# Kernel tuning notes

Measured on AMD Instinct MI355X. Metric: run time of the kernel, lower is better.

The kernel has to match this reference:

```python
import jax, jax.numpy as jnp
import numpy as np

NEG = -10000.0


def _build_label_vocab():
    vocab = {'O': 0}
    i = 1
    for t in ['PER', 'ORG', 'LOC', 'MISC']:
        for p in ['B', 'I', 'E', 'S']:
            vocab[f'{p}-{t}'] = i
            i += 1
    return vocab


def _init_transition(key):
    """Random transition with BIOES constraints, matching CRF.initialize()."""
    vocab = _build_label_vocab()
    L = len(vocab) + 2          # 19 (17 labels + start + end)
    start, end = L - 2, L - 1
    T = np.array(jax.random.normal(key, (L, L)), dtype=np.float32)
    T[:, end] = NEG
    T[start, :] = NEG
    for lf, i_f in vocab.items():
        pf, tf = ('O', 'O') if lf == 'O' else lf.split('-')
        for lt, i_t in vocab.items():
            pt, tt = ('O', 'O') if lt == 'O' else lt.split('-')
            allowed = (pf in ('O', 'E', 'S') and pt in ('O', 'B', 'S')) or \
                      (pf in ('B', 'I') and pt in ('I', 'E') and tf == tt)
            if not allowed:
                T[i_t, i_f] = NEG
    return jnp.asarray(T)


def setup_inputs() -> dict:
    key = jax.random.key(0)
    k1, k2, k3, k4 = jax.random.split(key, 4)
    B, S, NL = 4096, 256, 17
    logits = jax.random.normal(k1, (B, S, NL), dtype=jnp.float32)
    labels = jax.random.randint(k2, (B, S), 0, NL)
    lens = jax.random.randint(k3, (B,), 1, S + 1)   # lengths in [1, S]
    transition = _init_transition(k4)                # [19, 19]
    return {"logits": logits, "labels": labels, "lens": lens,
            "transition": transition}


def reference(logits, labels, lens, transition):
    """CRF log-likelihood: gold_score(pad_logits(logits)) - norm_score."""
    B, S, NL = logits.shape
    L = transition.shape[0]       # label_size = NL + 2
    start, end = L - 2, L - 1

    # pad_logits: append start/end columns with -10000
    pads = jnp.full((B, S, 2), NEG, dtype=logits.dtype)
    logits_p = jnp.concatenate([logits, pads], axis=2)   # [B, S, L]

    tmask = (jnp.arange(S)[None, :] < lens[:, None])     # [B, S] valid tokens

    # ---- gold score ----
    # unary: gather emission score of the gold label at each position
    unary = jnp.take_along_axis(logits_p, labels[:, :, None], axis=2)[:, :, 0]
    unary = (unary * tmask.astype(logits.dtype)).sum(axis=1)

    # binary: transition scores along the gold path (with start/end padding)
    labels_ext = jnp.concatenate(
        [jnp.full((B, 1), start, labels.dtype), labels,
         jnp.full((B, 1), end, labels.dtype)], axis=1)   # [B, S+2]
    emask = jnp.arange(S + 2)[None, :] < (lens + 1)[:, None]
    labels_ext = jnp.where(emask, labels_ext, end)
    trn_scr = transition[labels_ext[:, 1:], labels_ext[:, :-1]]  # [B, S+1]
    bmask = (jnp.arange(S + 1)[None, :] < (lens + 1)[:, None]).astype(logits.dtype)
    binary = (trn_scr * bmask).sum(axis=1)

    gold = unary + binary

    # ---- partition (norm) score: forward algorithm over time ----
    alpha0 = jnp.full((B, L), NEG, dtype=logits.dtype).at[:, start].set(0.0)

    def step(alpha, xs):
        logit, m = xs  # logit: [B, L], m: [B] bool (position < len)
        # alpha_nxt[b,i] = logit[b,i] + LSE_j(alpha[b,j] + T[i,j])
        nxt = logit + jax.nn.logsumexp(alpha[:, None, :] + transition[None], axis=2)
        alpha = jnp.where(m[:, None], nxt, alpha)
        return alpha, None

    alpha, _ = jax.lax.scan(step, alpha0,
                            (jnp.swapaxes(logits_p, 0, 1), tmask.T))
    alpha = alpha + transition[end][None, :]
    norm = jax.nn.logsumexp(alpha, axis=1)

    return gold - norm   # [B] per-sequence log-likelihood
```

## Files before the change

kernel.cpp:

```cpp
#include <hip/hip_runtime.h>

constexpr int S    = 256;
constexpr int NL   = 17;
constexpr int L    = 19;
constexpr int CAPB = 16384;

typedef float v4 __attribute__((ext_vector_type(4), aligned(4)));

__device__ float g_Z[CAPB * 17];
__device__ float g_V[CAPB * 17];
__device__ float g_mf[CAPB];
__device__ float g_mv[CAPB];

__host__ __device__ constexpr bool allowedTo(int i, int j) {
    const int pi = (i == 0) ? 4 : ((i - 1) & 3);
    const int pj = (j == 0) ? 4 : ((j - 1) & 3);
    const int ti = (i == 0) ? -1 : ((i - 1) >> 2);
    const int tj = (j == 0) ? -2 : ((j - 1) >> 2);
    const bool fromOES = (pj == 4) || (pj == 2) || (pj == 3);
    const bool toOBS   = (pi == 4) || (pi == 0) || (pi == 3);
    if (fromOES && toOBS) return true;
    if (((pj == 0) || (pj == 1)) && ((pi == 1) || (pi == 2)) && (ti == tj)) return true;
    return false;
}

#define STEP(T_, CUR, NXT, RN)                                              \
    {                                                                       \
        const int t_ = (T_);                                                \
        {                                                                   \
            const int o_ = tokoff(t_ + 1);                                  \
            const v4   l0 = *(const v4*)(base + o_);                        \
            const v4   l1 = *(const v4*)(base + o_ + 16);                   \
            const v4   l2 = *(const v4*)(base + o_ + 32);                   \
            const v4   l3 = *(const v4*)(base + o_ + 48);                   \
            const float l4 = *(const float*)(base + o_ + 64);               \
            NXT[0] = l0.x;  NXT[1] = l0.y;  NXT[2] = l0.z;  NXT[3] = l0.w;  \
            NXT[4] = l1.x;  NXT[5] = l1.y;  NXT[6] = l1.z;  NXT[7] = l1.w;  \
            NXT[8] = l2.x;  NXT[9] = l2.y;  NXT[10] = l2.z; NXT[11] = l2.w; \
            NXT[12] = l3.x; NXT[13] = l3.y; NXT[14] = l3.z; NXT[15] = l3.w; \
            NXT[16] = l4;                                                   \
        }                                                                   \
        float q[17];                                                        \
        _Pragma("unroll")                                                   \
        for (int j = 0; j < 17; ++j) q[j] = __expf(CUR[j]) * p[j];          \
        _Pragma("unroll")                                                   \
        for (int i = 0; i < 17; ++i) {                                      \
            float acc = 0.0f;                                               \
            bool  fst = true;                                               \
            _Pragma("unroll")                                               \
            for (int j = 0; j < 17; ++j) {                                  \
                const bool al = BWD ? allowedTo(j, i) : allowedTo(i, j);    \
                if (al) {                                                   \
                    acc = fst ? cf[i][j] * q[j]                             \
                              : fmaf(cf[i][j], q[j], acc);                  \
                    fst = false;                                            \
                }                                                           \
            }                                                               \
            p[i] = acc;                                                     \
        }                                                                   \
        if (RN) {                                                           \
            float mx = p[16];                                               \
            _Pragma("unroll")                                               \
            for (int i = 0; i < 16; i += 2)                                 \
                mx = fmaxf(mx, fmaxf(p[i], p[i + 1]));                      \
            const float r_ = __frcp_rn(mx);                                 \
            _Pragma("unroll")                                               \
            for (int i = 0; i < 17; ++i) p[i] *= r_;                        \
            m += __logf(mx);                                                \
        }                                                                   \
        if (t_ == nup - 1) {                                                \
            float* dst = SC + bc * 17;                                      \
            _Pragma("unroll")                                               \
            for (int i = 0; i < 17; ++i) dst[i] = p[i];                     \
            SM[bc] = m;                                                     \
        }                                                                   \
    }

template <bool BWD>
__device__ __forceinline__ void chain(const float* __restrict__ logits,
                                      const int*   __restrict__ lens,
                                      const float* __restrict__ T,
                                      int B, int z)
{
    const int  lane  = threadIdx.x;
    const int  braw  = z * 64 + lane;
    const bool valid = braw < B;
    const int  bc    = valid ? braw : 0;

    const int len = lens[bc];
    const int mid = len >> 1;
    int nup = BWD ? (len - 1 - mid) : mid;
    if (!valid) nup = 0;

    float cf[17][17];
    #pragma unroll
    for (int i = 0; i < 17; ++i)
        #pragma unroll
        for (int j = 0; j < 17; ++j) {
            const bool al = BWD ? allowedTo(j, i) : allowedTo(i, j);
            if (al) cf[i][j] = __expf(BWD ? T[j * L + i] : T[i * L + j]);
        }

    float p[17];
    #pragma unroll
    for (int i = 0; i < 17; ++i)
        p[i] = __expf(BWD ? T[(L - 1) * L + i] : T[i * L + (L - 2)]);

    float m = 0.0f;

    float* SC = BWD ? g_V : g_Z;
    float* SM = BWD ? g_mv : g_mf;

    if (nup == 0 && valid) {
        float* dst = SC + bc * 17;
        #pragma unroll
        for (int i = 0; i < 17; ++i) dst[i] = p[i];
        SM[bc] = 0.0f;
    }

    int nmax = nup;
    #pragma unroll
    for (int o = 32; o >= 1; o >>= 1) nmax = max(nmax, __shfl_xor(nmax, o));

    const char* base = (const char*)logits;
    const int   sb4  = bc * (S * NL * 4);

    auto tokoff = [&](int t) -> int {
        int tok = BWD ? (len - 1 - t) : t;
        if (BWD) tok = tok > 0 ? tok : 0;
        return sb4 + tok * (NL * 4);
    };

    float curv[17], nxtv[17];
    {
        const int o_ = tokoff(0);
        const v4   l0 = *(const v4*)(base + o_);
        const v4   l1 = *(const v4*)(base + o_ + 16);
        const v4   l2 = *(const v4*)(base + o_ + 32);
        const v4   l3 = *(const v4*)(base + o_ + 48);
        const float l4 = *(const float*)(base + o_ + 64);
        curv[0] = l0.x;  curv[1] = l0.y;  curv[2] = l0.z;  curv[3] = l0.w;
        curv[4] = l1.x;  curv[5] = l1.y;  curv[6] = l1.z;  curv[7] = l1.w;
        curv[8] = l2.x;  curv[9] = l2.y;  curv[10] = l2.z; curv[11] = l2.w;
        curv[12] = l3.x; curv[13] = l3.y; curv[14] = l3.z; curv[15] = l3.w;
        curv[16] = l4;
    }

    for (int tb = 0; tb < nmax; tb += 2) {
        STEP(tb,     curv, nxtv, false)
        STEP(tb + 1, nxtv, curv, ((tb & 3) == 2))
    }
}

__global__ __launch_bounds__(64, 1)
void crf_chain(const float* __restrict__ logits, const int* __restrict__ lens,
               const float* __restrict__ T, int B, int nbh)
{
    if ((int)blockIdx.x < nbh) chain<false>(logits, lens, T, B, blockIdx.x);
    else                       chain<true >(logits, lens, T, B, blockIdx.x - nbh);
}

__global__ __launch_bounds__(64)
void crf_combine(const float* __restrict__ logits, const int* __restrict__ labels,
                 const int* __restrict__ lens, const float* __restrict__ T,
                 float* __restrict__ out, int B)
{
    const int b    = blockIdx.x;
    const int wtid = threadIdx.x;
    const int len  = lens[b];
    const int mid  = len >> 1;

    float prod = 0.0f;
    if (wtid < 17) {
        const float z  = g_Z[b * 17 + wtid];
        const float v  = g_V[b * 17 + wtid];
        const float lg = logits[(size_t)b * (S * NL) + mid * NL + wtid];
        prod = z * v * __expf(lg);
    }
    #pragma unroll
    for (int o = 32; o >= 1; o >>= 1) prod += __shfl_xor(prod, o);
    const float norm = g_mf[b] + g_mv[b] + __logf(prod);

    const int* labp = labels + b * S;
    float gsum = 0.0f;
    for (int c = 0; c < len; c += 64) {
        const int tok = c + wtid;
        if (tok < len) {
            const int lab = labp[tok];
            const int prv = (tok == 0) ? (L - 2) : labp[tok - 1];
            gsum += logits[(size_t)b * (S * NL) + tok * NL + lab] + T[lab * L + prv];
        }
    }
    #pragma unroll
    for (int o = 32; o >= 1; o >>= 1) gsum += __shfl_xor(gsum, o);
    const float gold = gsum + T[(L - 1) * L + labp[len - 1]];

    if (wtid == 0) out[b] = gold - norm;
}

extern "C" void kernel_launch(void* const* d_in, const int* in_sizes, int n_in,
                              void* d_out, int out_size, void* d_ws, size_t ws_size,
                              hipStream_t stream)
{
    (void)n_in; (void)out_size; (void)d_ws; (void)ws_size;
    const float* logits     = (const float*)d_in[0];
    const int*   labels     = (const int*)d_in[1];
    const int*   lens       = (const int*)d_in[2];
    const float* transition = (const float*)d_in[3];
    float*       out        = (float*)d_out;
    const int B   = in_sizes[2];
    const int NBH = (B + 63) / 64;

    crf_chain<<<dim3(2 * NBH), dim3(64), 0, stream>>>(logits, lens, transition, B, NBH);
    crf_combine<<<dim3(B), dim3(64), 0, stream>>>(logits, labels, lens, transition, out, B);
}
```

Measured before the change: 166.5 us.

## Deepen logits prefetch to four tokens and hand-expand sparse CRF matvec

The forward and backward chain kernels now keep four token slots of logits in flight, which raises prefetch depth from one token to four so global load latency is hidden behind the serial recurrence. The sparse BIOES matvec is written out explicitly through macros and uses balanced tree additions in place of a serial FMA chain, which shortens each step's dependency chain. Renormalisation now runs once every four steps, and nmax is rounded up to a multiple of four. The cost is much higher register pressure from four slots plus the coefficients, and some extra padded iterations, with backward offsets clamped at the sequence start.

```diff
diff --git a/kernel.cpp b/kernel.cpp
--- a/kernel.cpp
+++ b/kernel.cpp
@@ -12,152 +12,197 @@
 __device__ float g_mf[CAPB];
 __device__ float g_mv[CAPB];
 
-__host__ __device__ constexpr bool allowedTo(int i, int j) {
-    const int pi = (i == 0) ? 4 : ((i - 1) & 3);
-    const int pj = (j == 0) ? 4 : ((j - 1) & 3);
-    const int ti = (i == 0) ? -1 : ((i - 1) >> 2);
-    const int tj = (j == 0) ? -2 : ((j - 1) >> 2);
-    const bool fromOES = (pj == 4) || (pj == 2) || (pj == 3);
-    const bool toOBS   = (pi == 4) || (pi == 0) || (pi == 3);
-    if (fromOES && toOBS) return true;
-    if (((pj == 0) || (pj == 1)) && ((pi == 1) || (pi == 2)) && (ti == tj)) return true;
-    return false;
-}
-
-#define STEP(T_, CUR, NXT, RN)                                              \
-    {                                                                       \
-        const int t_ = (T_);                                                \
-        {                                                                   \
-            const int o_ = tokoff(t_ + 1);                                  \
-            const v4   l0 = *(const v4*)(base + o_);                        \
-            const v4   l1 = *(const v4*)(base + o_ + 16);                   \
-            const v4   l2 = *(const v4*)(base + o_ + 32);                   \
-            const v4   l3 = *(const v4*)(base + o_ + 48);                   \
-            const float l4 = *(const float*)(base + o_ + 64);               \
-            NXT[0] = l0.x;  NXT[1] = l0.y;  NXT[2] = l0.z;  NXT[3] = l0.w;  \
-            NXT[4] = l1.x;  NXT[5] = l1.y;  NXT[6] = l1.z;  NXT[7] = l1.w;  \
-            NXT[8] = l2.x;  NXT[9] = l2.y;  NXT[10] = l2.z; NXT[11] = l2.w; \
-            NXT[12] = l3.x; NXT[13] = l3.y; NXT[14] = l3.z; NXT[15] = l3.w; \
-            NXT[16] = l4;                                                   \
-        }                                                                   \
-        float q[17];                                                        \
-        _Pragma("unroll")                                                   \
-        for (int j = 0; j < 17; ++j) q[j] = __expf(CUR[j]) * p[j];          \
-        _Pragma("unroll")                                                   \
-        for (int i = 0; i < 17; ++i) {                                      \
-            float acc = 0.0f;                                               \
-            bool  fst = true;                                               \
-            _Pragma("unroll")                                               \
-            for (int j = 0; j < 17; ++j) {                                  \
-                const bool al = BWD ? allowedTo(j, i) : allowedTo(i, j);    \
-                if (al) {                                                   \
-                    acc = fst ? cf[i][j] * q[j]                             \
-                              : fmaf(cf[i][j], q[j], acc);                  \
-                    fst = false;                                            \
-                }                                                           \
-            }                                                               \
-            p[i] = acc;                                                     \
-        }                                                                   \
-        if (RN) {                                                           \
-            float mx = p[16];                                               \
-            _Pragma("unroll")                                               \
-            for (int i = 0; i < 16; i += 2)                                 \
-                mx = fmaxf(mx, fmaxf(p[i], p[i + 1]));                      \
-            const float r_ = __frcp_rn(mx);                                 \
-            _Pragma("unroll")                                               \
-            for (int i = 0; i < 17; ++i) p[i] *= r_;                        \
-            m += __logf(mx);                                                \
-        }                                                                   \
-        if (t_ == nup - 1) {                                                \
-            float* dst = SC + bc * 17;                                      \
-            _Pragma("unroll")                                               \
-            for (int i = 0; i < 17; ++i) dst[i] = p[i];                     \
-            SM[bc] = m;                                                     \
-        }                                                                   \
-    }
-
-template <bool BWD>
-__device__ __forceinline__ void chain(const float* __restrict__ logits,
-                                      const int*   __restrict__ lens,
-                                      const float* __restrict__ T,
-                                      int B, int z)
+#define ROWF(X,i) X(i,0) X(i,3) X(i,4) X(i,7) X(i,8) X(i,11) X(i,12) X(i,15) X(i,16)
+#define FWD_ALL(X) \
+  ROWF(X,0) ROWF(X,1) ROWF(X,4) ROWF(X,5) ROWF(X,8) ROWF(X,9) ROWF(X,12) ROWF(X,13) ROWF(X,16) \
+  X(2,1) X(2,2) X(3,1) X(3,2) X(6,5) X(6,6) X(7,5) X(7,6) \
+  X(10,9) X(10,10) X(11,9) X(11,10) X(14,13) X(14,14) X(15,13) X(15,14)
+
+#define ROWB(X,i) X(i,0) X(i,1) X(i,4) X(i,5) X(i,8) X(i,9) X(i,12) X(i,13) X(i,16)
+#define BWD_ALL(X) \
+  ROWB(X,0) ROWB(X,3) ROWB(X,4) ROWB(X,7) ROWB(X,8) ROWB(X,11) ROWB(X,12) ROWB(X,15) ROWB(X,16) \
+  X(1,2) X(1,3) X(2,2) X(2,3) X(5,6) X(5,7) X(6,6) X(6,7) \
+  X(9,10) X(9,11) X(10,10) X(10,11) X(13,14) X(13,15) X(14,14) X(14,15)
+
+#define APPLY17(X) X(0) X(1) X(2) X(3) X(4) X(5) X(6) X(7) X(8) X(9) X(10) X(11) X(12) X(13) X(14) X(15) X(16)
+
+#define DCF_F(i,j) const float cf_##i##_##j = __expf(Tg[(i)*19+(j)]);
+#define DCF_B(i,j) const float cf_##i##_##j = __expf(Tg[(j)*19+(i)]);
+
+#define DPF(i) float p##i = __expf(Tg[(i)*19+17]);
+#define DPB(i) float p##i = __expf(Tg[18*19+(i)]);
+
+#define DECLSLOT(T) float T##0,T##1,T##2,T##3,T##4,T##5,T##6,T##7,T##8,T##9, \
+                          T##10,T##11,T##12,T##13,T##14,T##15,T##16;
+
+#define LOADTOK(T, OFF) { \
+    const char* a_ = base + (OFF); \
+    const v4 x0_ = *(const v4*)(a_); \
+    const v4 x1_ = *(const v4*)(a_ + 16); \
+    const v4 x2_ = *(const v4*)(a_ + 32); \
+    const v4 x3_ = *(const v4*)(a_ + 48); \
+    const float x4_ = *(const float*)(a_ + 64); \
+    T##0=x0_.x; T##1=x0_.y; T##2=x0_.z; T##3=x0_.w; \
+    T##4=x1_.x; T##5=x1_.y; T##6=x1_.z; T##7=x1_.w; \
+    T##8=x2_.x; T##9=x2_.y; T##10=x2_.z; T##11=x2_.w; \
+    T##12=x3_.x; T##13=x3_.y; T##14=x3_.z; T##15=x3_.w; T##16=x4_; }
+
+#define MKQALL(T) \
+    const float q0 = __expf(T##0) * p0;   const float q1 = __expf(T##1) * p1; \
+    const float q2 = __expf(T##2) * p2;   const float q3 = __expf(T##3) * p3; \
+    const float q4 = __expf(T##4) * p4;   const float q5 = __expf(T##5) * p5; \
+    const float q6 = __expf(T##6) * p6;   const float q7 = __expf(T##7) * p7; \
+    const float q8 = __expf(T##8) * p8;   const float q9 = __expf(T##9) * p9; \
+    const float q10 = __expf(T##10) * p10; const float q11 = __expf(T##11) * p11; \
+    const float q12 = __expf(T##12) * p12; const float q13 = __expf(T##13) * p13; \
+    const float q14 = __expf(T##14) * p14; const float q15 = __expf(T##15) * p15; \
+    const float q16 = __expf(T##16) * p16;
+
+#define FMQ(i,j) cf_##i##_##j * q##j
+#define ROW9N(i,a,b,c,d,e,f,g,h,k) \
+    const float n##i = (((FMQ(i,a)+FMQ(i,b)) + (FMQ(i,c)+FMQ(i,d))) + \
+                        ((FMQ(i,e)+FMQ(i,f)) + (FMQ(i,g)+FMQ(i,h)))) + FMQ(i,k);
+#define ROW2N(i,a,b) const float n##i = FMQ(i,a) + FMQ(i,b);
+
+#define MATVEC_F \
+    ROW9N(0,0,3,4,7,8,11,12,15,16)  ROW9N(1,0,3,4,7,8,11,12,15,16) \
+    ROW9N(4,0,3,4,7,8,11,12,15,16)  ROW9N(5,0,3,4,7,8,11,12,15,16) \
+    ROW9N(8,0,3,4,7,8,11,12,15,16)  ROW9N(9,0,3,4,7,8,11,12,15,16) \
+    ROW9N(12,0,3,4,7,8,11,12,15,16) ROW9N(13,0,3,4,7,8,11,12,15,16) \
+    ROW9N(16,0,3,4,7,8,11,12,15,16) \
+    ROW2N(2,1,2)   ROW2N(3,1,2)   ROW2N(6,5,6)   ROW2N(7,5,6) \
+    ROW2N(10,9,10) ROW2N(11,9,10) ROW2N(14,13,14) ROW2N(15,13,14)
+
+#define MATVEC_B \
+    ROW9N(0,0,1,4,5,8,9,12,13,16)  ROW9N(3,0,1,4,5,8,9,12,13,16) \
+    ROW9N(4,0,1,4,5,8,9,12,13,16)  ROW9N(7,0,1,4,5,8,9,12,13,16) \
+    ROW9N(8,0,1,4,5,8,9,12,13,16)  ROW9N(11,0,1,4,5,8,9,12,13,16) \
+    ROW9N(12,0,1,4,5,8,9,12,13,16) ROW9N(15,0,1,4,5,8,9,12,13,16) \
+    ROW9N(16,0,1,4,5,8,9,12,13,16) \
+    ROW2N(1,2,3)   ROW2N(2,2,3)   ROW2N(5,6,7)   ROW2N(6,6,7) \
+    ROW2N(9,10,11) ROW2N(10,10,11) ROW2N(13,14,15) ROW2N(14,14,15)
+
+#define ASG(i)  p##i = n##i;
+#define ASGR(i) p##i = n##i * r_;
+
+#define STORE_P { \
+    float* d_ = SC + bc * 17; \
+    d_[0]=p0; d_[1]=p1; d_[2]=p2; d_[3]=p3; d_[4]=p4; d_[5]=p5; d_[6]=p6; d_[7]=p7; \
+    d_[8]=p8; d_[9]=p9; d_[10]=p10; d_[11]=p11; d_[12]=p12; d_[13]=p13; d_[14]=p14; \
+    d_[15]=p15; d_[16]=p16; \
+    SM[bc] = m; }
+
+#define CHAINSTEP(T, T_, OFFV, RN, MV, DOCLAMP, SSTR) { \
+    MKQALL(T) \
+    OFFV += (SSTR); \
+    if (DOCLAMP) { if (OFFV < capLo) OFFV = capLo; } \
+    LOADTOK(T, OFFV) \
+    MV \
+    if (RN) { \
+        float mxA = fmaxf(fmaxf(n0,n1),  fmaxf(n2,n3)); \
+        float mxB = fmaxf(fmaxf(n4,n5),  fmaxf(n6,n7)); \
+        float mxC = fmaxf(fmaxf(n8,n9),  fmaxf(n10,n11)); \
+        float mxD = fmaxf(fmaxf(n12,n13),fmaxf(n14,n15)); \
+        float mx  = fmaxf(fmaxf(fmaxf(mxA,mxB), fmaxf(mxC,mxD)), n16); \
+        const float r_ = __frcp_rn(mx); \
+        m += __logf(mx); \
+        APPLY17(ASGR) \
+    } else { \
+        APPLY17(ASG) \
+    } \
+    if ((T_) == nup - 1) STORE_P \
+}
+
+__device__ __forceinline__ void chainF(const float* __restrict__ logits,
+                                       const int* __restrict__ lens,
+                                       const float* __restrict__ Tg, int B, int z)
 {
     const int  lane  = threadIdx.x;
     const int  braw  = z * 64 + lane;
     const bool valid = braw < B;
     const int  bc    = valid ? braw : 0;
-
-    const int len = lens[bc];
-    const int mid = len >> 1;
-    int nup = BWD ? (len - 1 - mid) : mid;
-    if (!valid) nup = 0;
-
-    float cf[17][17];
-    #pragma unroll
-    for (int i = 0; i < 17; ++i)
-        #pragma unroll
-        for (int j = 0; j < 17; ++j) {
-            const bool al = BWD ? allowedTo(j, i) : allowedTo(i, j);
-            if (al) cf[i][j] = __expf(BWD ? T[j * L + i] : T[i * L + j]);
-        }
-
-    float p[17];
-    #pragma unroll
-    for (int i = 0; i < 17; ++i)
-        p[i] = __expf(BWD ? T[(L - 1) * L + i] : T[i * L + (L - 2)]);
-
-    float m = 0.0f;
-
-    float* SC = BWD ? g_V : g_Z;
-    float* SM = BWD ? g_mv : g_mf;
-
-    if (nup == 0 && valid) {
-        float* dst = SC + bc * 17;
-        #pragma unroll
-        for (int i = 0; i < 17; ++i) dst[i] = p[i];
-        SM[bc] = 0.0f;
-    }
+    const int  len   = lens[bc];
+    const int  mid   = len >> 1;
+    const int  nup   = valid ? mid : 0;
+
+    FWD_ALL(DCF_F)
+    APPLY17(DPF)
+    float  m  = 0.0f;
+    float* SC = g_Z;
+    float* SM = g_mf;
+    if (nup == 0 && valid) STORE_P
 
     int nmax = nup;
     #pragma unroll
     for (int o = 32; o >= 1; o >>= 1) nmax = max(nmax, __shfl_xor(nmax, o));
-
-    const char* base = (const char*)logits;
-    const int   sb4  = bc * (S * NL * 4);
-
-    auto tokoff = [&](int t) -> int {
-        int tok = BWD ? (len - 1 - t) : t;
-        if (BWD) tok = tok > 0 ? tok : 0;
-        return sb4 + tok * (NL * 4);
-    };
-
-    float curv[17], nxtv[17];
-    {
-        const int o_ = tokoff(0);
-        const v4   l0 = *(const v4*)(base + o_);
-        const v4   l1 = *(const v4*)(base + o_ + 16);
-        const v4   l2 = *(const v4*)(base + o_ + 32);
-        const v4   l3 = *(const v4*)(base + o_ + 48);
-        const float l4 = *(const float*)(base + o_ + 64);
-        curv[0] = l0.x;  curv[1] = l0.y;  curv[2] = l0.z;  curv[3] = l0.w;
-        curv[4] = l1.x;  curv[5] = l1.y;  curv[6] = l1.z;  curv[7] = l1.w;
-        curv[8] = l2.x;  curv[9] = l2.y;  curv[10] = l2.z; curv[11] = l2.w;
-        curv[12] = l3.x; curv[13] = l3.y; curv[14] = l3.z; curv[15] = l3.w;
-        curv[16] = l4;
-    }
-
-    for (int tb = 0; tb < nmax; tb += 2) {
-        STEP(tb,     curv, nxtv, false)
-        STEP(tb + 1, nxtv, curv, ((tb & 3) == 2))
+    nmax = (nmax + 3) & ~3;
+
+    const char* base  = (const char*)logits;
+    const int   sb4   = bc * (S * NL * 4);
+    const int   capLo = sb4;
+    int off0 = sb4, off1 = sb4 + 68, off2 = sb4 + 136, off3 = sb4 + 204;
+
+    DECLSLOT(sA) DECLSLOT(sB) DECLSLOT(sC) DECLSLOT(sD)
+    LOADTOK(sA, off0) LOADTOK(sB, off1) LOADTOK(sC, off2) LOADTOK(sD, off3)
+
+    for (int tb = 0; tb < nmax; tb += 4) {
+        CHAINSTEP(sA, tb,     off0, 0, MATVEC_F, 0, 272)
+        CHAINSTEP(sB, tb + 1, off1, 0, MATVEC_F, 0, 272)
+        CHAINSTEP(sC, tb + 2, off2, 0, MATVEC_F, 0, 272)
+        CHAINSTEP(sD, tb + 3, off3, 1, MATVEC_F, 0, 272)
+    }
+}
+
+__device__ __forceinline__ void chainB(const float* __restrict__ logits,
+                                       const int* __restrict__ lens,
+                                       const float* __restrict__ Tg, int B, int z)
+{
+    const int  lane  = threadIdx.x;
+    const int  braw  = z * 64 + lane;
+    const bool valid = braw < B;
+    const int  bc    = valid ? braw : 0;
+    const int  len   = lens[bc];
+    const int  mid   = len >> 1;
+    const int  nup   = valid ? (len - 1 - mid) : 0;
+
+    BWD_ALL(DCF_B)
+    APPLY17(DPB)
+    float  m  = 0.0f;
+    float* SC = g_V;
+    float* SM = g_mv;
+    if (nup == 0 && valid) STORE_P
+
+    int nmax = nup;
+    #pragma unroll
+    for (int o = 32; o >= 1; o >>= 1) nmax = max(nmax, __shfl_xor(nmax, o));
+    nmax = (nmax + 3) & ~3;
+
+    const char* base  = (const char*)logits;
+    const int   sb4   = bc * (S * NL * 4);
+    const int   capLo = sb4;
+    const int   t0    = len - 1;
+    int off0 = sb4 + max(t0,     0) * 68;
+    int off1 = sb4 + max(t0 - 1, 0) * 68;
+    int off2 = sb4 + max(t0 - 2, 0) * 68;
+    int off3 = sb4 + max(t0 - 3, 0) * 68;
+
+    DECLSLOT(sA) DECLSLOT(sB) DECLSLOT(sC) DECLSLOT(sD)
+    LOADTOK(sA, off0) LOADTOK(sB, off1) LOADTOK(sC, off2) LOADTOK(sD, off3)
+
+    for (int tb = 0; tb < nmax; tb += 4) {
+        CHAINSTEP(sA, tb,     off0, 0, MATVEC_B, 1, -272)
+        CHAINSTEP(sB, tb + 1, off1, 0, MATVEC_B, 1, -272)
+        CHAINSTEP(sC, tb + 2, off2, 0, MATVEC_B, 1, -272)
+        CHAINSTEP(sD, tb + 3, off3, 1, MATVEC_B, 1, -272)
     }
 }
 
 __global__ __launch_bounds__(64, 1)
 void crf_chain(const float* __restrict__ logits, const int* __restrict__ lens,
-               const float* __restrict__ T, int B, int nbh)
-{
-    if ((int)blockIdx.x < nbh) chain<false>(logits, lens, T, B, blockIdx.x);
-    else                       chain<true >(logits, lens, T, B, blockIdx.x - nbh);
+               const float* __restrict__ Tg, int B, int nbh)
+{
+    if ((int)blockIdx.x < nbh) chainF(logits, lens, Tg, B, blockIdx.x);
+    else                       chainB(logits, lens, Tg, B, blockIdx.x - nbh);
 }
 
 __global__ __launch_bounds__(64)
```

Measured after the change: 168.0 us. About the same (+0.9%).

## Split each CRF chain across two lanes with shuffle-exchanged partial states

Applied to the files above, without the earlier changes.

Each sequence's forward and backward recurrence is now handled by a pair of lanes, each holding 9 of the 17 states. The states are grouped so that only 5 boundary values per lane are exchanged with __shfl_xor each step, and the sparse BIOES transition structure is exploited with small dense A/B blocks and 2-term updates. Loads go through a four-deep rotating slot buffer of per-token logits, and renormalisation happens every four steps. This doubles the number of waves and halves the per-lane serial work and register pressure, at the cost of extra cross-lane shuffles on the critical path.

```diff
diff --git a/kernel.cpp b/kernel.cpp
--- a/kernel.cpp
+++ b/kernel.cpp
@@ -12,152 +12,156 @@
 __device__ float g_mf[CAPB];
 __device__ float g_mv[CAPB];
 
-__host__ __device__ constexpr bool allowedTo(int i, int j) {
-    const int pi = (i == 0) ? 4 : ((i - 1) & 3);
-    const int pj = (j == 0) ? 4 : ((j - 1) & 3);
-    const int ti = (i == 0) ? -1 : ((i - 1) >> 2);
-    const int tj = (j == 0) ? -2 : ((j - 1) >> 2);
-    const bool fromOES = (pj == 4) || (pj == 2) || (pj == 3);
-    const bool toOBS   = (pi == 4) || (pi == 0) || (pi == 3);
-    if (fromOES && toOBS) return true;
-    if (((pj == 0) || (pj == 1)) && ((pi == 1) || (pi == 2)) && (ti == tj)) return true;
-    return false;
-}
-
-#define STEP(T_, CUR, NXT, RN)                                              \
-    {                                                                       \
-        const int t_ = (T_);                                                \
-        {                                                                   \
-            const int o_ = tokoff(t_ + 1);                                  \
-            const v4   l0 = *(const v4*)(base + o_);                        \
-            const v4   l1 = *(const v4*)(base + o_ + 16);                   \
-            const v4   l2 = *(const v4*)(base + o_ + 32);                   \
-            const v4   l3 = *(const v4*)(base + o_ + 48);                   \
-            const float l4 = *(const float*)(base + o_ + 64);               \
-            NXT[0] = l0.x;  NXT[1] = l0.y;  NXT[2] = l0.z;  NXT[3] = l0.w;  \
-            NXT[4] = l1.x;  NXT[5] = l1.y;  NXT[6] = l1.z;  NXT[7] = l1.w;  \
-            NXT[8] = l2.x;  NXT[9] = l2.y;  NXT[10] = l2.z; NXT[11] = l2.w; \
-            NXT[12] = l3.x; NXT[13] = l3.y; NXT[14] = l3.z; NXT[15] = l3.w; \
-            NXT[16] = l4;                                                   \
-        }                                                                   \
-        float q[17];                                                        \
-        _Pragma("unroll")                                                   \
-        for (int j = 0; j < 17; ++j) q[j] = __expf(CUR[j]) * p[j];          \
-        _Pragma("unroll")                                                   \
-        for (int i = 0; i < 17; ++i) {                                      \
-            float acc = 0.0f;                                               \
-            bool  fst = true;                                               \
-            _Pragma("unroll")                                               \
-            for (int j = 0; j < 17; ++j) {                                  \
-                const bool al = BWD ? allowedTo(j, i) : allowedTo(i, j);    \
-                if (al) {                                                   \
-                    acc = fst ? cf[i][j] * q[j]                             \
-                              : fmaf(cf[i][j], q[j], acc);                  \
-                    fst = false;                                            \
-                }                                                           \
-            }                                                               \
-            p[i] = acc;                                                     \
-        }                                                                   \
-        if (RN) {                                                           \
-            float mx = p[16];                                               \
-            _Pragma("unroll")                                               \
-            for (int i = 0; i < 16; i += 2)                                 \
-                mx = fmaxf(mx, fmaxf(p[i], p[i + 1]));                      \
-            const float r_ = __frcp_rn(mx);                                 \
-            _Pragma("unroll")                                               \
-            for (int i = 0; i < 17; ++i) p[i] *= r_;                        \
-            m += __logf(mx);                                                \
-        }                                                                   \
-        if (t_ == nup - 1) {                                                \
-            float* dst = SC + bc * 17;                                      \
-            _Pragma("unroll")                                               \
-            for (int i = 0; i < 17; ++i) dst[i] = p[i];                     \
-            SM[bc] = m;                                                     \
-        }                                                                   \
-    }
-
-template <bool BWD>
-__device__ __forceinline__ void chain(const float* __restrict__ logits,
-                                      const int*   __restrict__ lens,
-                                      const float* __restrict__ T,
-                                      int B, int z)
-{
-    const int  lane  = threadIdx.x;
-    const int  braw  = z * 64 + lane;
+
+#define CSTEP2(SL, TT, OFFV, RN) { \
+    float q[9]; \
+    _Pragma("unroll") for (int j = 0; j < 9; ++j) q[j] = __expf(SL[j]) * p[j]; \
+    OFFV += ADV; \
+    if (BWD) OFFV = OFFV < sb4 ? sb4 : OFFV; \
+    loadSlot(SL, OFFV); \
+    float ow[5], rv[5]; \
+    _Pragma("unroll") for (int i = 0; i < 5; ++i) ow[i] = q[Ee[i]]; \
+    _Pragma("unroll") for (int i = 0; i < 5; ++i) rv[i] = __shfl_xor(ow[i], 1); \
+    float N[9]; \
+    _Pragma("unroll") for (int r = 0; r < 5; ++r) { \
+        float a = A[r][0] * ow[0]; \
+        _Pragma("unroll") for (int i = 1; i < 5; ++i) a = fmaf(A[r][i], ow[i], a); \
+        _Pragma("unroll") for (int i = 0; i < 5; ++i) a = fmaf(Bc[r][i], rv[i], a); \
+        N[WO[r]] = a; \
+    } \
+    _Pragma("unroll") for (int r = 0; r < 4; ++r) \
+        N[NO[r]] = fmaf(NC[r][1], q[NIb[r]], NC[r][0] * q[NIa[r]]); \
+    if (RN) { \
+        float mx = N[0]; \
+        _Pragma("unroll") for (int j = 1; j < 9; ++j) mx = fmaxf(mx, N[j]); \
+        mx = fmaxf(mx, __shfl_xor(mx, 1)); \
+        const float rr = __frcp_rn(mx); \
+        m += __logf(mx); \
+        _Pragma("unroll") for (int j = 0; j < 9; ++j) p[j] = N[j] * rr; \
+    } else { \
+        _Pragma("unroll") for (int j = 0; j < 9; ++j) p[j] = N[j]; \
+    } \
+    if ((TT) == nup - 1) storeP(); \
+}
+
+template <int BWD>
+__device__ __forceinline__ void chain2(const float* __restrict__ logits,
+                                       const int* __restrict__ lens,
+                                       const float* __restrict__ Tg, int B, int z)
+{
+    const int  wtid  = threadIdx.x;
+    const int  P     = wtid & 1;
+    const int  braw  = z * 32 + (wtid >> 1);
     const bool valid = braw < B;
     const int  bc    = valid ? braw : 0;
-
-    const int len = lens[bc];
-    const int mid = len >> 1;
-    int nup = BWD ? (len - 1 - mid) : mid;
-    if (!valid) nup = 0;
-
-    float cf[17][17];
-    #pragma unroll
-    for (int i = 0; i < 17; ++i)
+    const int  len   = lens[bc];
+    const int  mid   = len >> 1;
+    const int  nup   = valid ? (BWD ? (len - 1 - mid) : mid) : 0;
+
+    constexpr int Ee[5]  = {0, BWD ? 1 : 3, 4, BWD ? 5 : 7, 8};
+    constexpr int WO[5]  = {0, BWD ? 3 : 1, 4, BWD ? 7 : 5, 8};
+    constexpr int NO[4]  = {BWD ? 1 : 2, BWD ? 2 : 3, BWD ? 5 : 6, BWD ? 6 : 7};
+    constexpr int NIa[4] = {BWD ? 2 : 1, BWD ? 2 : 1, BWD ? 6 : 5, BWD ? 6 : 5};
+    constexpr int NIb[4] = {BWD ? 3 : 2, BWD ? 3 : 2, BWD ? 7 : 6, BWD ? 7 : 6};
+
+    auto stOf = [&](int par, int j) -> int {
+        return par ? (8 + j) : (j < 8 ? j : -1);
+    };
+    auto expT = [&](int r, int c) -> float {
+        return __expf(BWD ? Tg[c * 19 + r] : Tg[r * 19 + c]);
+    };
+
+    float A[5][5], Bc[5][5], NC[4][2];
+    #pragma unroll
+    for (int r = 0; r < 5; ++r) {
+        const int rw  = stOf(P, WO[r]);
+        const int rwc = rw < 0 ? 0 : rw;
         #pragma unroll
-        for (int j = 0; j < 17; ++j) {
-            const bool al = BWD ? allowedTo(j, i) : allowedTo(i, j);
-            if (al) cf[i][j] = __expf(BWD ? T[j * L + i] : T[i * L + j]);
+        for (int i = 0; i < 5; ++i) {
+            const int sa = stOf(P, Ee[i]);
+            const int sb = stOf(1 - P, Ee[i]);
+            A[r][i]  = (rw >= 0 && sa >= 0) ? expT(rwc, sa < 0 ? 0 : sa) : 0.0f;
+            Bc[r][i] = (rw >= 0 && sb >= 0) ? expT(rwc, sb < 0 ? 0 : sb) : 0.0f;
         }
-
-    float p[17];
-    #pragma unroll
-    for (int i = 0; i < 17; ++i)
-        p[i] = __expf(BWD ? T[(L - 1) * L + i] : T[i * L + (L - 2)]);
-
+    }
+    #pragma unroll
+    for (int r = 0; r < 4; ++r) {
+        const int rn = stOf(P, NO[r]);
+        NC[r][0] = expT(rn, stOf(P, NIa[r]));
+        NC[r][1] = expT(rn, stOf(P, NIb[r]));
+    }
+
+    float p[9];
+    #pragma unroll
+    for (int j = 0; j < 9; ++j) {
+        const int s  = stOf(P, j);
+        const int sc = s < 0 ? 0 : s;
+        p[j] = s < 0 ? 0.0f
+                     : __expf(BWD ? Tg[18 * 19 + sc] : Tg[sc * 19 + 17]);
+    }
     float m = 0.0f;
 
     float* SC = BWD ? g_V : g_Z;
     float* SM = BWD ? g_mv : g_mf;
-
-    if (nup == 0 && valid) {
-        float* dst = SC + bc * 17;
+    auto storeP = [&]() {
+        float* d_ = SC + bc * 17 + (P ? 8 : 0);
         #pragma unroll
-        for (int i = 0; i < 17; ++i) dst[i] = p[i];
-        SM[bc] = 0.0f;
-    }
+        for (int j = 0; j < 9; ++j)
+            if (j < 8 || P) d_[j] = p[j];
+        if (P) SM[bc] = m;
+    };
+
+    if (nup == 0 && valid) storeP();
 
     int nmax = nup;
     #pragma unroll
     for (int o = 32; o >= 1; o >>= 1) nmax = max(nmax, __shfl_xor(nmax, o));
-
-    const char* base = (const char*)logits;
-    const int   sb4  = bc * (S * NL * 4);
-
-    auto tokoff = [&](int t) -> int {
-        int tok = BWD ? (len - 1 - t) : t;
-        if (BWD) tok = tok > 0 ? tok : 0;
-        return sb4 + tok * (NL * 4);
-    };
-
-    float curv[17], nxtv[17];
-    {
-        const int o_ = tokoff(0);
-        const v4   l0 = *(const v4*)(base + o_);
-        const v4   l1 = *(const v4*)(base + o_ + 16);
-        const v4   l2 = *(const v4*)(base + o_ + 32);
-        const v4   l3 = *(const v4*)(base + o_ + 48);
-        const float l4 = *(const float*)(base + o_ + 64);
-        curv[0] = l0.x;  curv[1] = l0.y;  curv[2] = l0.z;  curv[3] = l0.w;
-        curv[4] = l1.x;  curv[5] = l1.y;  curv[6] = l1.z;  curv[7] = l1.w;
-        curv[8] = l2.x;  curv[9] = l2.y;  curv[10] = l2.z; curv[11] = l2.w;
-        curv[12] = l3.x; curv[13] = l3.y; curv[14] = l3.z; curv[15] = l3.w;
-        curv[16] = l4;
-    }
-
-    for (int tb = 0; tb < nmax; tb += 2) {
-        STEP(tb,     curv, nxtv, false)
-        STEP(tb + 1, nxtv, curv, ((tb & 3) == 2))
+    nmax = (nmax + 3) & ~3;
+
+    const char* baseb = (const char*)logits;
+    const int   sb4   = bc * (S * NL * 4);
+    const int   ADV   = BWD ? -272 : 272;
+    const int   poff  = P ? 32 : 0;
+
+    auto loadSlot = [&](float (&sl)[9], int off) {
+        const char* a  = baseb + off + poff;
+        const v4    x0 = *(const v4*)(a);
+        const v4    x1 = *(const v4*)(a + 16);
+        const float x2 = *(const float*)(baseb + off + (P ? 64 : 0));
+        sl[0] = x0.x; sl[1] = x0.y; sl[2] = x0.z; sl[3] = x0.w;
+        sl[4] = x1.x; sl[5] = x1.y; sl[6] = x1.z; sl[7] = x1.w;
+        sl[8] = P ? x2 : 0.0f;
+    };
+
+    int offA, offB2, offC, offD;
+    if (BWD) {
+        const int t0 = len - 1;
+        offA  = sb4 + max(t0,     0) * 68;
+        offB2 = sb4 + max(t0 - 1, 0) * 68;
+        offC  = sb4 + max(t0 - 2, 0) * 68;
+        offD  = sb4 + max(t0 - 3, 0) * 68;
+    } else {
+        offA = sb4; offB2 = sb4 + 68; offC = sb4 + 136; offD = sb4 + 204;
+    }
+
+    float slA[9], slB[9], slC[9], slD[9];
+    loadSlot(slA, offA); loadSlot(slB, offB2);
+    loadSlot(slC, offC); loadSlot(slD, offD);
+
+    for (int tb = 0; tb < nmax; tb += 4) {
+        CSTEP2(slA, tb,     offA,  0)
+        CSTEP2(slB, tb + 1, offB2, 0)
+        CSTEP2(slC, tb + 2, offC,  0)
+        CSTEP2(slD, tb + 3, offD,  1)
     }
 }
 
 __global__ __launch_bounds__(64, 1)
 void crf_chain(const float* __restrict__ logits, const int* __restrict__ lens,
-               const float* __restrict__ T, int B, int nbh)
-{
-    if ((int)blockIdx.x < nbh) chain<false>(logits, lens, T, B, blockIdx.x);
-    else                       chain<true >(logits, lens, T, B, blockIdx.x - nbh);
+               const float* __restrict__ Tg, int B, int nz)
+{
+    if ((int)blockIdx.x < nz) chain2<0>(logits, lens, Tg, B, blockIdx.x);
+    else                      chain2<1>(logits, lens, Tg, B, blockIdx.x - nz);
 }
 
 __global__ __launch_bounds__(64)
@@ -208,9 +212,9 @@
     const int*   lens       = (const int*)d_in[2];
     const float* transition = (const float*)d_in[3];
     float*       out        = (float*)d_out;
-    const int B   = in_sizes[2];
-    const int NBH = (B + 63) / 64;
-
-    crf_chain<<<dim3(2 * NBH), dim3(64), 0, stream>>>(logits, lens, transition, B, NBH);
+    const int B  = in_sizes[2];
+    const int NZ = (B + 31) / 32;
+
+    crf_chain<<<dim3(2 * NZ), dim3(64), 0, stream>>>(logits, lens, transition, B, NZ);
     crf_combine<<<dim3(B), dim3(64), 0, stream>>>(logits, labels, lens, transition, out, B);
 }
```

Result: faster. 148.4 us (-10.9%).
